# Performance work log

Hardware: AMD Instinct MI355X
Metric: run time of the kernel (lower is better)

## Reference

```python
import jax, jax.numpy as jnp
import numpy as np
from functools import partial

B, C, H, W = 32, 16, 256, 256
HIDDEN = 128
N_FILT = 3

SOBEL_X = jnp.array([[-1., 0., 1.], [-2., 0., 2.], [-1., 0., 1.]], dtype=jnp.float32)
SOBEL_Y = jnp.array([[-1., -2., -1.], [0., 0., 0.], [1., 2., 1.]], dtype=jnp.float32)
CELL_ID = jnp.array([[0., 0., 0.], [0., 1., 0.], [0., 0., 0.]], dtype=jnp.float32)
ALIVE_K = jnp.ones((1, 1, 3, 3), dtype=jnp.float32)


def _conv3x3_same(x, kernel):
    # x: [B, Cin, H, W], kernel: [Cout, Cin, 3, 3], padding=1
    return jax.lax.conv_general_dilated(
        x, kernel, window_strides=(1, 1), padding='SAME',
        dimension_numbers=('NCHW', 'OIHW', 'NCHW'))


def _perceive(x, k2d):
    # Original weight is k2d repeated to [16,16,3,3] (identical kernel for every
    # in/out channel pair), so conv2d(x, W) == conv2d(sum_c x_c, k2d) broadcast
    # to 16 identical output channels. Same math, far less work.
    xs = jnp.sum(x, axis=1, keepdims=True)            # [B,1,H,W]
    out = _conv3x3_same(xs, k2d[None, None, :, :])     # [B,1,H,W]
    return jnp.broadcast_to(out, (x.shape[0], C, x.shape[2], x.shape[3]))


def setup_inputs() -> dict:
    key = jax.random.key(0)
    k1, k2, k3 = jax.random.split(key, 3)
    x = jax.random.uniform(k1, (B, C, H, W), dtype=jnp.float32)
    random_mask = jax.random.randint(k2, (B, 1, H, W), 0, 2, dtype=jnp.int32)
    w1 = jax.random.normal(k3, (HIDDEN, N_FILT * C), dtype=jnp.float32) * 0.05
    b1 = jnp.zeros((HIDDEN,), dtype=jnp.float32)
    # NOTE: original inits fc2.weight to zeros; use small random so dx is nontrivial
    w2 = jax.random.normal(jax.random.fold_in(key, 7), (C, HIDDEN), dtype=jnp.float32) * 0.05
    b2 = jnp.zeros((C,), dtype=jnp.float32)
    return {'x': x, 'random_mask': random_mask, 'w1': w1, 'b1': b1, 'w2': w2, 'b2': b2}


def reference(x, random_mask, w1, b1, w2, b2):
    # perception: [sobelX, sobelY, cellId] blocks of 16 channels each -> [B,48,H,W]
    perception = jnp.concatenate(
        [_perceive(x, SOBEL_X), _perceive(x, SOBEL_Y), _perceive(x, CELL_ID)], axis=1)
    # 1x1 conv MLP
    h = jnp.einsum('oc,bchw->bohw', w1, perception) + b1[None, :, None, None]
    h = jax.nn.relu(h)
    dx = jnp.einsum('oc,bchw->bohw', w2, h) + b2[None, :, None, None]
    # stochastic update: mask broadcast over all 16 channels
    x_new = x + dx * random_mask.astype(x.dtype)
    # alive mask: 3x3 ones conv over (alpha > 0.1), then > 0, broadcast over channels
    alpha_alive = (x_new[:, 3:4, :, :] > 0.1).astype(x.dtype)  # [B,1,H,W]
    alive = _conv3x3_same(alpha_alive, ALIVE_K) > 0.0           # [B,1,H,W] bool
    return x_new * alive.astype(x.dtype)
```

## Files before the change

### kernel.cpp

```cpp
#include <hip/hip_runtime.h>
#include <hip/hip_bf16.h>

#define B_   32
#define C_   16
#define H_   256
#define W_   256
#define HW_  65536
#define HID_ 128
#define T_   4
#define NBLK_ (B_*H_/T_)

typedef __attribute__((ext_vector_type(8))) short bf16x8;
typedef __attribute__((ext_vector_type(4))) float f32x4;

__device__ __forceinline__ short f2bf(float f) {
    __hip_bfloat16 h = __float2bfloat16(f);
    return __builtin_bit_cast(short, h);
}

__device__ __forceinline__ int cvt_pk_bf16(float lo, float hi) {
    int r;
    asm("v_cvt_pk_bf16_f32 %0, %1, %2" : "=v"(r) : "v"(lo), "v"(hi));
    return r;
}

__global__ __launch_bounds__(128) void nca_prep(
    const float* __restrict__ w1, const float* __restrict__ b1,
    float4* __restrict__ coef4)
{
    int o = threadIdx.x;
    float A = 0.f, Bc = 0.f, Cc = 0.f;
    #pragma unroll
    for (int k = 0;  k < 16; ++k) A  += w1[o*48 + k];
    #pragma unroll
    for (int k = 16; k < 32; ++k) Bc += w1[o*48 + k];
    #pragma unroll
    for (int k = 32; k < 48; ++k) Cc += w1[o*48 + k];
    coef4[o] = make_float4(A, Bc, Cc, b1[o]);
}

__global__ __launch_bounds__(256, 4) void nca_fused(
    const float* __restrict__ x, const int* __restrict__ mask,
    const float4* __restrict__ coef4, const float* __restrict__ w2,
    const float* __restrict__ b2,
    float* __restrict__ out, unsigned char* __restrict__ alpha)
{
    __shared__ float srow[T_+2][W_];
    __shared__ short hlds[4*2048];
    __shared__ short w2lds[4*64*8];

    const int tid  = threadIdx.x;
    const int lane = tid & 63;
    const int widx = tid >> 6;
    const int col  = tid;
    const int q = lane & 15;
    const int g = lane >> 4;

    const int blk = blockIdx.x;
    const int b   = blk >> 6;
    const int r0  = (blk & 63) * T_;

    const float* xb = x    + (size_t)b * C_ * HW_;
    const int*   mb = mask + (size_t)b * HW_;
    float*       ob = (float*)out + (size_t)b * C_ * HW_;
    unsigned char* ab = alpha + (size_t)b * HW_;

    {
        const int kb = tid >> 6, l = tid & 63;
        const int qq = l & 15, gg = l >> 4;
        const float* wp = w2 + qq*HID_ + kb*32 + gg*8;
        bf16x8 a;
        #pragma unroll
        for (int j = 0; j < 8; ++j) a[j] = f2bf(wp[j]);
        *(bf16x8*)(w2lds + tid*8) = a;
    }

    f32x4 bias;
    #pragma unroll
    for (int r = 0; r < 4; ++r) bias[r] = b2[g*4 + r];

    const int wswz = (lane ^ (lane >> 2)) & 3;
    const int rsw  = (q ^ (q >> 2)) & 3;
    short* hw = hlds + widx*2048;

    float xnext[C_];
    {
        float s0 = 0.f;
        if (r0 > 0) {
            #pragma unroll
            for (int c = 0; c < C_; ++c)
                s0 += xb[c*HW_ + (r0-1)*W_ + col];
        }
        float s1 = 0.f;
        #pragma unroll
        for (int c = 0; c < C_; ++c)
            s1 += xb[c*HW_ + r0*W_ + col];
        #pragma unroll
        for (int c = 0; c < C_; ++c)
            xnext[c] = xb[c*HW_ + (r0+1)*W_ + col];
        srow[0][col] = s0;
        srow[1][col] = s1;
    }

    for (int r = 0; r < T_; ++r) {
        const int row = r0 + r;

        {
            float s = 0.f;
            #pragma unroll
            for (int c = 0; c < C_; ++c) s += xnext[c];
            srow[r+2][col] = s;
        }
        __syncthreads();

        if (r < T_-1) {
            const int nr = r0 + r + 2;
            if (nr < H_) {
                #pragma unroll
                for (int c = 0; c < C_; ++c)
                    xnext[c] = xb[c*HW_ + nr*W_ + col];
            } else {
                #pragma unroll
                for (int c = 0; c < C_; ++c) xnext[c] = 0.f;
            }
        }

        const int pstrip = row*W_ + (widx << 6);
        float mv[4];
        #pragma unroll
        for (int t = 0; t < 4; ++t)
            mv[t] = (float)mb[pstrip + t*16 + q];

        const bool jm = col > 0, jp = col < W_-1;
        const float* sA = srow[r];
        const float* sB = srow[r+1];
        const float* sC = srow[r+2];
        float n00 = jm ? sA[col-1] : 0.f, n01 = sA[col], n02 = jp ? sA[col+1] : 0.f;
        float n10 = jm ? sB[col-1] : 0.f, n11 = sB[col], n12 = jp ? sB[col+1] : 0.f;
        float n20 = jm ? sC[col-1] : 0.f, n21 = sC[col], n22 = jp ? sC[col+1] : 0.f;
        float px = (n02 - n00) + 2.f*(n12 - n10) + (n22 - n20);
        float py = (n20 - n00) + 2.f*(n21 - n01) + (n22 - n02);
        float sc = n11;

        f32x4 acc[4];
        #pragma unroll
        for (int t = 0; t < 4; ++t) acc[t] = bias;

        #pragma unroll
        for (int kb = 0; kb < 4; ++kb) {
            #pragma unroll
            for (int c = 0; c < 4; ++c) {
                float h[8];
                #pragma unroll
                for (int u = 0; u < 8; ++u) {
                    const float4 cf = coef4[kb*32 + c*8 + u];
                    h[u] = fmaxf(fmaf(cf.x, px, fmaf(cf.y, py, fmaf(cf.z, sc, cf.w))), 0.f);
                }
                int4 hd = make_int4(cvt_pk_bf16(h[0], h[1]), cvt_pk_bf16(h[2], h[3]),
                                    cvt_pk_bf16(h[4], h[5]), cvt_pk_bf16(h[6], h[7]));
                *(int4*)(hw + lane*32 + ((c ^ wswz) << 3)) = hd;
            }
            __builtin_amdgcn_wave_barrier();
            bf16x8 af = *(const bf16x8*)(w2lds + (kb*64 + lane)*8);
            #pragma unroll
            for (int t = 0; t < 4; ++t) {
                const int pp = t*16 + q;
                bf16x8 bfrag = *(const bf16x8*)(hw + pp*32 + (((g ^ rsw) & 3) << 3));
                acc[t] = __builtin_amdgcn_mfma_f32_16x16x32_bf16(
                             af, bfrag, acc[t], 0, 0, 0);
            }
            __builtin_amdgcn_wave_barrier();
        }

        #pragma unroll
        for (int t = 0; t < 4; ++t) {
            const int pp = pstrip + t*16 + q;
            float xn3 = 0.f;
            #pragma unroll
            for (int e = 0; e < 4; ++e) {
                const int ch = g*4 + e;
                float xv = xb[ch*HW_ + pp];
                float xn = fmaf(acc[t][e], mv[t], xv);
                ob[ch*HW_ + pp] = xn;
                if (ch == 3) xn3 = xn;
            }
            if (g == 0) ab[pp] = (xn3 > 0.1f) ? (unsigned char)1
                                              : (unsigned char)0;
        }
    }
}

__global__ __launch_bounds__(256) void nca_alive(
    const unsigned char* __restrict__ alpha, float* __restrict__ out)
{
    int t = blockIdx.x * blockDim.x + threadIdx.x;
    if (t >= B_*HW_) return;
    int b = t >> 16;
    int p = t & (HW_-1);
    int i = p >> 8;
    int j = p & (W_-1);
    const unsigned char* ab = alpha + (size_t)b * HW_;

    bool im = i > 0, ip = i < H_-1, jm = j > 0, jp = j < W_-1;
    int acc = ab[p];
    acc += jm ? ab[p-1] : 0;
    acc += jp ? ab[p+1] : 0;
    if (im) {
        acc += ab[p-W_];
        acc += jm ? ab[p-W_-1] : 0;
        acc += jp ? ab[p-W_+1] : 0;
    }
    if (ip) {
        acc += ab[p+W_];
        acc += jm ? ab[p+W_-1] : 0;
        acc += jp ? ab[p+W_+1] : 0;
    }
    if (acc == 0) {
        size_t base = (size_t)b * C_ * HW_ + p;
        #pragma unroll
        for (int c = 0; c < C_; ++c) out[base + (size_t)c * HW_] = 0.f;
    }
}

extern "C" void kernel_launch(void* const* d_in, const int* in_sizes, int n_in,
                              void* d_out, int out_size, void* d_ws, size_t ws_size,
                              hipStream_t stream)
{
    const float* x    = (const float*)d_in[0];
    const int*   mask = (const int*)d_in[1];
    const float* w1   = (const float*)d_in[2];
    const float* b1   = (const float*)d_in[3];
    const float* w2   = (const float*)d_in[4];
    const float* b2   = (const float*)d_in[5];
    float* out = (float*)d_out;

    char* ws = (char*)d_ws;
    unsigned char* alpha = (unsigned char*)ws;
    float4*        coef4 = (float4*)(ws + (size_t)B_*HW_);

    nca_prep<<<1, 128, 0, stream>>>(w1, b1, coef4);

    nca_fused<<<NBLK_, 256, 0, stream>>>(x, mask, coef4, w2, b2, out, alpha);

    int n = B_*HW_;
    nca_alive<<<(n + 255)/256, 256, 0, stream>>>(alpha, out);
}
```

Baseline: 97.58 us.

## Compute hidden layer with MFMA instead of scalar FMAs, double rows per block

The first 1x1 layer (3 perception features plus bias to 128 hidden units) moves from per-lane scalar FMA loops over coef4 to 32x32x16 bf16 MFMA. The perception vector is packed into bf16 B-fragments through a small LDS staging area, and ReLU'd outputs are written into the swizzled hidden tile for the second MFMA. w1 coefficients and w2 fragments are preloaded into registers once per block. Rows per block rise from 4 to 8, which amortizes the halo loads. The risks are bf16 rounding of the perception values and coefficients, extra LDS traffic, and fewer blocks for occupancy.

```diff
diff --git a/kernel.cpp b/kernel.cpp
--- a/kernel.cpp
+++ b/kernel.cpp
@@ -7,11 +7,12 @@
 #define W_   256
 #define HW_  65536
 #define HID_ 128
-#define T_   4
+#define T_   8
 #define NBLK_ (B_*H_/T_)
 
-typedef __attribute__((ext_vector_type(8))) short bf16x8;
-typedef __attribute__((ext_vector_type(4))) float f32x4;
+typedef __attribute__((ext_vector_type(8)))  short bf16x8;
+typedef __attribute__((ext_vector_type(4)))  float f32x4;
+typedef __attribute__((ext_vector_type(16))) float f32x16;
 
 __device__ __forceinline__ short f2bf(float f) {
     __hip_bfloat16 h = __float2bfloat16(f);
@@ -48,17 +49,22 @@
     __shared__ float srow[T_+2][W_];
     __shared__ short hlds[4*2048];
     __shared__ short w2lds[4*64*8];
+    __shared__ short w1lds[4*32*4];
+    __shared__ int   vlds[4*64*2];
 
     const int tid  = threadIdx.x;
     const int lane = tid & 63;
     const int widx = tid >> 6;
     const int col  = tid;
-    const int q = lane & 15;
-    const int g = lane >> 4;
+    const int q  = lane & 15;
+    const int g  = lane >> 4;
+    const int cl = lane & 31;
+    const int hi = lane >> 5;
+    const int usw = cl & 6;
 
     const int blk = blockIdx.x;
-    const int b   = blk >> 6;
-    const int r0  = (blk & 63) * T_;
+    const int b   = blk >> 5;
+    const int r0  = (blk & 31) * T_;
 
     const float* xb = x    + (size_t)b * C_ * HW_;
     const int*   mb = mask + (size_t)b * HW_;
@@ -74,33 +80,45 @@
         for (int j = 0; j < 8; ++j) a[j] = f2bf(wp[j]);
         *(bf16x8*)(w2lds + tid*8) = a;
     }
-
-    f32x4 bias;
-    #pragma unroll
-    for (int r = 0; r < 4; ++r) bias[r] = b2[g*4 + r];
-
-    const int wswz = (lane ^ (lane >> 2)) & 3;
-    const int rsw  = (q ^ (q >> 2)) & 3;
-    short* hw = hlds + widx*2048;
+    if (tid < 128) {
+        const float4 cf = coef4[tid];
+        *(int2*)(w1lds + tid*4) = make_int2(cvt_pk_bf16(cf.x, cf.y),
+                                            cvt_pk_bf16(cf.z, cf.w));
+    }
 
     float xnext[C_];
     {
         float s0 = 0.f;
         if (r0 > 0) {
             #pragma unroll
-            for (int c = 0; c < C_; ++c)
-                s0 += xb[c*HW_ + (r0-1)*W_ + col];
+            for (int c = 0; c < C_; ++c) s0 += xb[c*HW_ + (r0-1)*W_ + col];
         }
         float s1 = 0.f;
         #pragma unroll
-        for (int c = 0; c < C_; ++c)
-            s1 += xb[c*HW_ + r0*W_ + col];
-        #pragma unroll
-        for (int c = 0; c < C_; ++c)
-            xnext[c] = xb[c*HW_ + (r0+1)*W_ + col];
+        for (int c = 0; c < C_; ++c) s1 += xb[c*HW_ + r0*W_ + col];
+        #pragma unroll
+        for (int c = 0; c < C_; ++c) xnext[c] = xb[c*HW_ + (r0+1)*W_ + col];
         srow[0][col] = s0;
         srow[1][col] = s1;
     }
+    __syncthreads();
+
+    int2 a1[4];
+    #pragma unroll
+    for (int ch = 0; ch < 4; ++ch) a1[ch] = *(const int2*)(w1lds + (ch*32 + cl)*4);
+    bf16x8 af2[4];
+    #pragma unroll
+    for (int kb = 0; kb < 4; ++kb) af2[kb] = *(const bf16x8*)(w2lds + (kb*64 + lane)*8);
+    f32x4 bias;
+    #pragma unroll
+    for (int r = 0; r < 4; ++r) bias[r] = b2[g*4 + r];
+
+    const bool lo = (lane < 32);
+    int* vt = vlds + widx*128;
+    char* hb = (char*)(hlds + widx*2048);
+
+    f32x16 z16 = {0.f,0.f,0.f,0.f,0.f,0.f,0.f,0.f,
+                  0.f,0.f,0.f,0.f,0.f,0.f,0.f,0.f};
 
     for (int r = 0; r < T_; ++r) {
         const int row = r0 + r;
@@ -117,8 +135,7 @@
             const int nr = r0 + r + 2;
             if (nr < H_) {
                 #pragma unroll
-                for (int c = 0; c < C_; ++c)
-                    xnext[c] = xb[c*HW_ + nr*W_ + col];
+                for (int c = 0; c < C_; ++c) xnext[c] = xb[c*HW_ + nr*W_ + col];
             } else {
                 #pragma unroll
                 for (int c = 0; c < C_; ++c) xnext[c] = 0.f;
@@ -128,46 +145,60 @@
         const int pstrip = row*W_ + (widx << 6);
         float mv[4];
         #pragma unroll
-        for (int t = 0; t < 4; ++t)
-            mv[t] = (float)mb[pstrip + t*16 + q];
+        for (int t = 0; t < 4; ++t) mv[t] = (float)mb[pstrip + t*16 + q];
 
         const bool jm = col > 0, jp = col < W_-1;
         const float* sA = srow[r];
         const float* sB = srow[r+1];
         const float* sC = srow[r+2];
         float n00 = jm ? sA[col-1] : 0.f, n01 = sA[col], n02 = jp ? sA[col+1] : 0.f;
-        float n10 = jm ? sB[col-1] : 0.f, n11 = sB[col], n12 = jp ? sB[col+1] : 0.f;
+        float n10 = jm ? sB[col-1] : 0.f,                n12 = jp ? sB[col+1] : 0.f;
         float n20 = jm ? sC[col-1] : 0.f, n21 = sC[col], n22 = jp ? sC[col+1] : 0.f;
         float px = (n02 - n00) + 2.f*(n12 - n10) + (n22 - n20);
         float py = (n20 - n00) + 2.f*(n21 - n01) + (n22 - n02);
-        float sc = n11;
+        float sc = sB[col];
+
+        *(int2*)(vt + lane*2) = make_int2(cvt_pk_bf16(px, py), cvt_pk_bf16(sc, 1.f));
+        __builtin_amdgcn_wave_barrier();
+
+        int2 v0 = *(const int2*)(vt + cl*2);
+        int2 v1 = *(const int2*)(vt + (32 + cl)*2);
+        int4 b0i = make_int4(lo ? v0.x : 0, lo ? v0.y : 0, 0, 0);
+        int4 b1i = make_int4(lo ? v1.x : 0, lo ? v1.y : 0, 0, 0);
+        bf16x8 bf0 = __builtin_bit_cast(bf16x8, b0i);
+        bf16x8 bf1 = __builtin_bit_cast(bf16x8, b1i);
 
         f32x4 acc[4];
         #pragma unroll
         for (int t = 0; t < 4; ++t) acc[t] = bias;
 
         #pragma unroll
-        for (int kb = 0; kb < 4; ++kb) {
-            #pragma unroll
-            for (int c = 0; c < 4; ++c) {
-                float h[8];
-                #pragma unroll
-                for (int u = 0; u < 8; ++u) {
-                    const float4 cf = coef4[kb*32 + c*8 + u];
-                    h[u] = fmaxf(fmaf(cf.x, px, fmaf(cf.y, py, fmaf(cf.z, sc, cf.w))), 0.f);
-                }
-                int4 hd = make_int4(cvt_pk_bf16(h[0], h[1]), cvt_pk_bf16(h[2], h[3]),
-                                    cvt_pk_bf16(h[4], h[5]), cvt_pk_bf16(h[6], h[7]));
-                *(int4*)(hw + lane*32 + ((c ^ wswz) << 3)) = hd;
+        for (int ch = 0; ch < 4; ++ch) {
+            int4 ai = make_int4(lo ? a1[ch].x : 0, lo ? a1[ch].y : 0, 0, 0);
+            bf16x8 afr = __builtin_bit_cast(bf16x8, ai);
+            f32x16 p0 = __builtin_amdgcn_mfma_f32_32x32x16_bf16(afr, bf0, z16, 0, 0, 0);
+            f32x16 p1 = __builtin_amdgcn_mfma_f32_32x32x16_bf16(afr, bf1, z16, 0, 0, 0);
+
+            #pragma unroll
+            for (int m = 0; m < 4; ++m) {
+                const int sl = ((2*m + hi) ^ usw) << 3;
+                int2 d0 = make_int2(
+                    cvt_pk_bf16(fmaxf(p0[4*m+0],0.f), fmaxf(p0[4*m+1],0.f)),
+                    cvt_pk_bf16(fmaxf(p0[4*m+2],0.f), fmaxf(p0[4*m+3],0.f)));
+                *(int2*)(hb + cl*64 + sl) = d0;
+                int2 d1 = make_int2(
+                    cvt_pk_bf16(fmaxf(p1[4*m+0],0.f), fmaxf(p1[4*m+1],0.f)),
+                    cvt_pk_bf16(fmaxf(p1[4*m+2],0.f), fmaxf(p1[4*m+3],0.f)));
+                *(int2*)(hb + (32+cl)*64 + sl) = d1;
             }
             __builtin_amdgcn_wave_barrier();
-            bf16x8 af = *(const bf16x8*)(w2lds + (kb*64 + lane)*8);
+
             #pragma unroll
             for (int t = 0; t < 4; ++t) {
                 const int pp = t*16 + q;
-                bf16x8 bfrag = *(const bf16x8*)(hw + pp*32 + (((g ^ rsw) & 3) << 3));
+                bf16x8 hbf = *(const bf16x8*)(hb + pp*64 + (((2*g) ^ (pp & 6)) << 3));
                 acc[t] = __builtin_amdgcn_mfma_f32_16x16x32_bf16(
-                             af, bfrag, acc[t], 0, 0, 0);
+                             af2[ch], hbf, acc[t], 0, 0, 0);
             }
             __builtin_amdgcn_wave_barrier();
         }
@@ -178,11 +209,11 @@
             float xn3 = 0.f;
             #pragma unroll
             for (int e = 0; e < 4; ++e) {
-                const int ch = g*4 + e;
-                float xv = xb[ch*HW_ + pp];
+                const int chn = g*4 + e;
+                float xv = xb[chn*HW_ + pp];
                 float xn = fmaf(acc[t][e], mv[t], xv);
-                ob[ch*HW_ + pp] = xn;
-                if (ch == 3) xn3 = xn;
+                ob[chn*HW_ + pp] = xn;
+                if (chn == 3) xn3 = xn;
             }
             if (g == 0) ab[pp] = (xn3 > 0.1f) ? (unsigned char)1
                                               : (unsigned char)0;
```

After: 187.9 us. +92.5%, slower.

## Compute hidden layer in packed fp16, use fp16 MFMA, double rows per block

Applied to the files above, without the earlier changes.

Replaces the scalar fp32 FMA hidden-layer computation with packed fp16x2 FMAs (v_pk_fma_f16 style), halving VALU instructions for the 128-wide hidden activation, and switches the MFMA and W2 operands from bf16 to fp16. W2 fragments are now hoisted into registers once per block instead of reloaded from LDS each row. Rows per block increase from 4 to 8, amortizing halo loads and W2 setup. This lowers hidden-layer precision to fp16 (coefficients, pre-activation), risks overflow/precision drift, and halves the grid size.

```diff
diff --git a/kernel.cpp b/kernel.cpp
--- a/kernel.cpp
+++ b/kernel.cpp
@@ -1,5 +1,5 @@
 #include <hip/hip_runtime.h>
-#include <hip/hip_bf16.h>
+#include <hip/hip_fp16.h>
 
 #define B_   32
 #define C_   16
@@ -7,27 +7,25 @@
 #define W_   256
 #define HW_  65536
 #define HID_ 128
-#define T_   4
+#define T_   8
 #define NBLK_ (B_*H_/T_)
 
-typedef __attribute__((ext_vector_type(8))) short bf16x8;
-typedef __attribute__((ext_vector_type(4))) float f32x4;
-
-__device__ __forceinline__ short f2bf(float f) {
-    __hip_bfloat16 h = __float2bfloat16(f);
-    return __builtin_bit_cast(short, h);
-}
-
-__device__ __forceinline__ int cvt_pk_bf16(float lo, float hi) {
-    int r;
-    asm("v_cvt_pk_bf16_f32 %0, %1, %2" : "=v"(r) : "v"(lo), "v"(hi));
-    return r;
+typedef __attribute__((ext_vector_type(8))) _Float16 f16x8;
+typedef __attribute__((ext_vector_type(2))) _Float16 f16x2;
+typedef __attribute__((ext_vector_type(4))) float    f32x4;
+
+__device__ __forceinline__ int h2i(f16x2 h) { return __builtin_bit_cast(int, h); }
+__device__ __forceinline__ f16x2 i2h(int i) { return __builtin_bit_cast(f16x2, i); }
+
+__device__ __forceinline__ f16x2 pk(float a, float b) {
+    f16x2 r; r.x = (_Float16)a; r.y = (_Float16)b; return r;
 }
 
 __global__ __launch_bounds__(128) void nca_prep(
     const float* __restrict__ w1, const float* __restrict__ b1,
-    float4* __restrict__ coef4)
-{
+    int4* __restrict__ coefH)
+{
+    __shared__ float4 tmp[128];
     int o = threadIdx.x;
     float A = 0.f, Bc = 0.f, Cc = 0.f;
     #pragma unroll
@@ -36,12 +34,18 @@
     for (int k = 16; k < 32; ++k) Bc += w1[o*48 + k];
     #pragma unroll
     for (int k = 32; k < 48; ++k) Cc += w1[o*48 + k];
-    coef4[o] = make_float4(A, Bc, Cc, b1[o]);
+    tmp[o] = make_float4(A, Bc, Cc, b1[o]);
+    __syncthreads();
+    if (o < 64) {
+        float4 e = tmp[2*o], f = tmp[2*o+1];
+        coefH[o] = make_int4(h2i(pk(e.x, f.x)), h2i(pk(e.y, f.y)),
+                             h2i(pk(e.z, f.z)), h2i(pk(e.w, f.w)));
+    }
 }
 
 __global__ __launch_bounds__(256, 4) void nca_fused(
     const float* __restrict__ x, const int* __restrict__ mask,
-    const float4* __restrict__ coef4, const float* __restrict__ w2,
+    const int4* __restrict__ coefH, const float* __restrict__ w2,
     const float* __restrict__ b2,
     float* __restrict__ out, unsigned char* __restrict__ alpha)
 {
@@ -57,8 +61,8 @@
     const int g = lane >> 4;
 
     const int blk = blockIdx.x;
-    const int b   = blk >> 6;
-    const int r0  = (blk & 63) * T_;
+    const int b   = blk >> 5;
+    const int r0  = (blk & 31) * T_;
 
     const float* xb = x    + (size_t)b * C_ * HW_;
     const int*   mb = mask + (size_t)b * HW_;
@@ -69,38 +73,39 @@
         const int kb = tid >> 6, l = tid & 63;
         const int qq = l & 15, gg = l >> 4;
         const float* wp = w2 + qq*HID_ + kb*32 + gg*8;
-        bf16x8 a;
-        #pragma unroll
-        for (int j = 0; j < 8; ++j) a[j] = f2bf(wp[j]);
-        *(bf16x8*)(w2lds + tid*8) = a;
-    }
-
-    f32x4 bias;
-    #pragma unroll
-    for (int r = 0; r < 4; ++r) bias[r] = b2[g*4 + r];
-
-    const int wswz = (lane ^ (lane >> 2)) & 3;
-    const int rsw  = (q ^ (q >> 2)) & 3;
-    short* hw = hlds + widx*2048;
+        f16x8 a;
+        #pragma unroll
+        for (int j = 0; j < 8; ++j) a[j] = (_Float16)wp[j];
+        *(f16x8*)(w2lds + tid*8) = a;
+    }
 
     float xnext[C_];
     {
         float s0 = 0.f;
         if (r0 > 0) {
             #pragma unroll
-            for (int c = 0; c < C_; ++c)
-                s0 += xb[c*HW_ + (r0-1)*W_ + col];
+            for (int c = 0; c < C_; ++c) s0 += xb[c*HW_ + (r0-1)*W_ + col];
         }
         float s1 = 0.f;
         #pragma unroll
-        for (int c = 0; c < C_; ++c)
-            s1 += xb[c*HW_ + r0*W_ + col];
-        #pragma unroll
-        for (int c = 0; c < C_; ++c)
-            xnext[c] = xb[c*HW_ + (r0+1)*W_ + col];
+        for (int c = 0; c < C_; ++c) s1 += xb[c*HW_ + r0*W_ + col];
+        #pragma unroll
+        for (int c = 0; c < C_; ++c) xnext[c] = xb[c*HW_ + (r0+1)*W_ + col];
         srow[0][col] = s0;
         srow[1][col] = s1;
     }
+    __syncthreads();
+
+    f16x8 af2[4];
+    #pragma unroll
+    for (int kb = 0; kb < 4; ++kb) af2[kb] = *(const f16x8*)(w2lds + (kb*64 + lane)*8);
+    f32x4 bias;
+    #pragma unroll
+    for (int r = 0; r < 4; ++r) bias[r] = b2[g*4 + r];
+
+    const int wswz = (lane ^ (lane >> 2)) & 3;
+    const int rsw  = (q ^ (q >> 2)) & 3;
+    short* hw = hlds + widx*2048;
 
     for (int r = 0; r < T_; ++r) {
         const int row = r0 + r;
@@ -117,8 +122,7 @@
             const int nr = r0 + r + 2;
             if (nr < H_) {
                 #pragma unroll
-                for (int c = 0; c < C_; ++c)
-                    xnext[c] = xb[c*HW_ + nr*W_ + col];
+                for (int c = 0; c < C_; ++c) xnext[c] = xb[c*HW_ + nr*W_ + col];
             } else {
                 #pragma unroll
                 for (int c = 0; c < C_; ++c) xnext[c] = 0.f;
@@ -128,19 +132,23 @@
         const int pstrip = row*W_ + (widx << 6);
         float mv[4];
         #pragma unroll
-        for (int t = 0; t < 4; ++t)
-            mv[t] = (float)mb[pstrip + t*16 + q];
+        for (int t = 0; t < 4; ++t) mv[t] = (float)mb[pstrip + t*16 + q];
 
         const bool jm = col > 0, jp = col < W_-1;
         const float* sA = srow[r];
         const float* sB = srow[r+1];
         const float* sC = srow[r+2];
         float n00 = jm ? sA[col-1] : 0.f, n01 = sA[col], n02 = jp ? sA[col+1] : 0.f;
-        float n10 = jm ? sB[col-1] : 0.f, n11 = sB[col], n12 = jp ? sB[col+1] : 0.f;
+        float n10 = jm ? sB[col-1] : 0.f,                n12 = jp ? sB[col+1] : 0.f;
         float n20 = jm ? sC[col-1] : 0.f, n21 = sC[col], n22 = jp ? sC[col+1] : 0.f;
         float px = (n02 - n00) + 2.f*(n12 - n10) + (n22 - n20);
         float py = (n20 - n00) + 2.f*(n21 - n01) + (n22 - n02);
-        float sc = n11;
+        float sc = sB[col];
+
+        const f16x2 px2 = pk(px, px);
+        const f16x2 py2 = pk(py, py);
+        const f16x2 sc2 = pk(sc, sc);
+        const f16x2 z2  = pk(0.f, 0.f);
 
         f32x4 acc[4];
         #pragma unroll
@@ -150,24 +158,27 @@
         for (int kb = 0; kb < 4; ++kb) {
             #pragma unroll
             for (int c = 0; c < 4; ++c) {
-                float h[8];
+                int hd[4];
                 #pragma unroll
-                for (int u = 0; u < 8; ++u) {
-                    const float4 cf = coef4[kb*32 + c*8 + u];
-                    h[u] = fmaxf(fmaf(cf.x, px, fmaf(cf.y, py, fmaf(cf.z, sc, cf.w))), 0.f);
+                for (int u = 0; u < 4; ++u) {
+                    const int4 cw = coefH[kb*16 + c*4 + u];
+                    f16x2 h2 = __builtin_elementwise_fma(i2h(cw.x), px2,
+                               __builtin_elementwise_fma(i2h(cw.y), py2,
+                               __builtin_elementwise_fma(i2h(cw.z), sc2,
+                                                         i2h(cw.w))));
+                    h2 = __builtin_elementwise_max(h2, z2);
+                    hd[u] = h2i(h2);
                 }
-                int4 hd = make_int4(cvt_pk_bf16(h[0], h[1]), cvt_pk_bf16(h[2], h[3]),
-                                    cvt_pk_bf16(h[4], h[5]), cvt_pk_bf16(h[6], h[7]));
-                *(int4*)(hw + lane*32 + ((c ^ wswz) << 3)) = hd;
+                *(int4*)(hw + lane*32 + ((c ^ wswz) << 3)) =
+                    make_int4(hd[0], hd[1], hd[2], hd[3]);
             }
             __builtin_amdgcn_wave_barrier();
-            bf16x8 af = *(const bf16x8*)(w2lds + (kb*64 + lane)*8);
             #pragma unroll
             for (int t = 0; t < 4; ++t) {
                 const int pp = t*16 + q;
-                bf16x8 bfrag = *(const bf16x8*)(hw + pp*32 + (((g ^ rsw) & 3) << 3));
-                acc[t] = __builtin_amdgcn_mfma_f32_16x16x32_bf16(
-                             af, bfrag, acc[t], 0, 0, 0);
+                f16x8 hbf = *(const f16x8*)(hw + pp*32 + (((g ^ rsw) & 3) << 3));
+                acc[t] = __builtin_amdgcn_mfma_f32_16x16x32_f16(
+                             af2[kb], hbf, acc[t], 0, 0, 0);
             }
             __builtin_amdgcn_wave_barrier();
         }
@@ -178,11 +189,11 @@
             float xn3 = 0.f;
             #pragma unroll
             for (int e = 0; e < 4; ++e) {
-                const int ch = g*4 + e;
-                float xv = xb[ch*HW_ + pp];
+                const int chn = g*4 + e;
+                float xv = xb[chn*HW_ + pp];
                 float xn = fmaf(acc[t][e], mv[t], xv);
-                ob[ch*HW_ + pp] = xn;
-                if (ch == 3) xn3 = xn;
+                ob[chn*HW_ + pp] = xn;
+                if (chn == 3) xn3 = xn;
             }
             if (g == 0) ab[pp] = (xn3 > 0.1f) ? (unsigned char)1
                                               : (unsigned char)0;
@@ -236,11 +247,11 @@
 
     char* ws = (char*)d_ws;
     unsigned char* alpha = (unsigned char*)ws;
-    float4*        coef4 = (float4*)(ws + (size_t)B_*HW_);
-
-    nca_prep<<<1, 128, 0, stream>>>(w1, b1, coef4);
-
-    nca_fused<<<NBLK_, 256, 0, stream>>>(x, mask, coef4, w2, b2, out, alpha);
+    int4*          coefH = (int4*)(ws + (size_t)B_*HW_);
+
+    nca_prep<<<1, 128, 0, stream>>>(w1, b1, coefH);
+
+    nca_fused<<<NBLK_, 256, 0, stream>>>(x, mask, coefH, w2, b2, out, alpha);
 
     int n = B_*HW_;
     nca_alive<<<(n + 255)/256, 256, 0, stream>>>(alpha, out);
```

Measured after the change: 117.4 us. 20.3% more time.
